# Kernel tuning notes

Measured on AMD Instinct MI355X. Metric: run time of the kernel, lower is better.

Reference implementation:

```python
import jax, jax.numpy as jnp
import numpy as np

N = 40000   # num nodes
C = 128     # in_channels
H = 8       # num_heads
D = C // H  # head_dim = 16
E = 640000  # num edges
FF = 4 * C


def layer_norm(x, g, b, eps=1e-5):
    m = jnp.mean(x, axis=-1, keepdims=True)
    v = jnp.mean((x - m) ** 2, axis=-1, keepdims=True)
    return (x - m) / jnp.sqrt(v + eps) * g + b


def setup_inputs() -> dict:
    key = jax.random.key(0)
    ks = jax.random.split(key, 16)
    s = 0.02
    x = jax.random.normal(ks[0], (N, C), dtype=jnp.float32)
    edge_index = jax.random.randint(ks[1], (2, E), 0, N, dtype=jnp.int64)
    return {
        'x': x,
        'edge_index': edge_index,
        'Wq': jax.random.normal(ks[2], (C, C), jnp.float32) * s,
        'bq': jnp.zeros((C,), jnp.float32),
        'Wk': jax.random.normal(ks[3], (C, C), jnp.float32) * s,
        'bk': jnp.zeros((C,), jnp.float32),
        'Wv': jax.random.normal(ks[4], (C, C), jnp.float32) * s,
        'bv': jnp.zeros((C,), jnp.float32),
        'Wo': jax.random.normal(ks[5], (C, C), jnp.float32) * s,
        'bo': jnp.zeros((C,), jnp.float32),
        'ln1_g': jnp.ones((C,), jnp.float32),
        'ln1_b': jnp.zeros((C,), jnp.float32),
        'ln2_g': jnp.ones((C,), jnp.float32),
        'ln2_b': jnp.zeros((C,), jnp.float32),
        'W1': jax.random.normal(ks[6], (C, FF), jnp.float32) * s,
        'b1': jnp.zeros((FF,), jnp.float32),
        'W2': jax.random.normal(ks[7], (FF, C), jnp.float32) * s,
        'b2': jnp.zeros((C,), jnp.float32),
    }


def reference(x, edge_index, Wq, bq, Wk, bk, Wv, bv, Wo, bo,
              ln1_g, ln1_b, ln2_g, ln2_b, W1, b1, W2, b2):
    residual = x
    xn = layer_norm(x, ln1_g, ln1_b)
    q = (xn @ Wq + bq).reshape(N, H, D)
    k = (xn @ Wk + bk).reshape(N, H, D)
    v = (xn @ Wv + bv).reshape(N, H, D)
    src, dst = edge_index[0], edge_index[1]
    # per-edge scores: [E, H]
    scores = jnp.einsum('ehd,ehd->eh', q[dst], k[src]) / jnp.sqrt(jnp.float32(D))
    # NOTE: faithful to the source — softmax over ALL edges (dim=0), not per-destination
    attn = jax.nn.softmax(scores, axis=0)[:, :, None]          # [E, H, 1]
    weighted = v[src] * attn                                   # [E, H, D]
    aggregated = jax.ops.segment_sum(weighted, dst, num_segments=N)  # [N, H, D]
    out = aggregated.reshape(N, C) @ Wo + bo
    x1 = residual + out
    residual2 = x1
    xn2 = layer_norm(x1, ln2_g, ln2_b)
    ffn = jax.nn.relu(xn2 @ W1 + b1) @ W2 + b2
    return residual2 + ffn
```

## Files before the change

kernel.cpp:

```cpp
#include <hip/hip_runtime.h>
#include <math.h>

#define NNODES 40000
#define CCH    128
#define NH     8
#define HD     16
#define NEDGE  640000
#define NBLK   157
#define FBLK   10000
#define RBLK   40

typedef __attribute__((ext_vector_type(8))) short bf16x8;
typedef __attribute__((ext_vector_type(4))) float f32x4;
typedef __attribute__((ext_vector_type(2))) float f32x2;

__device__ inline unsigned short f2bf(float f) {
  union { float f; unsigned u; } c; c.f = f;
  unsigned r = c.u + 0x7fffu + ((c.u >> 16) & 1u);
  return (unsigned short)(r >> 16);
}
__device__ inline float bfs(unsigned short u) { union { unsigned i; float f; } c; c.i = (unsigned)u << 16; return c.f; }
__device__ inline float bflo(unsigned u) { union { unsigned i; float f; } c; c.i = u << 16; return c.f; }
__device__ inline float bfhi(unsigned u) { union { unsigned i; float f; } c; c.i = u & 0xffff0000u; return c.f; }

__device__ inline unsigned char f2fp8(float v) {
#if __has_builtin(__builtin_amdgcn_cvt_pk_fp8_f32)
  return (unsigned char)(__builtin_amdgcn_cvt_pk_fp8_f32(v, v, 0, false) & 0xff);
#else
  union { float f; unsigned u; } c; c.f = v;
  unsigned s = (c.u >> 24) & 0x80;
  int e = (int)((c.u >> 23) & 0xff) - 127;
  unsigned m = c.u & 0x7fffff;
  if (e > 8) return s | 0x7e;
  if (e >= -6) {
    unsigned q = (m + 0x80000) >> 20; unsigned ee = e + 7;
    if (q == 8) { q = 0; ee++; }
    if (ee > 15) return s | 0x7e;
    return s | (ee << 3) | q;
  }
  if (e < -10) return (unsigned char)s;
  float a = fabsf(v); unsigned q = (unsigned)(a * 512.f + 0.5f); if (q > 7) q = 7;
  return s | q;
#endif
}
__device__ inline void fp8x4d(unsigned w, float* o) {
#if __has_builtin(__builtin_amdgcn_cvt_pk_f32_fp8)
  f32x2 lo = __builtin_amdgcn_cvt_pk_f32_fp8((int)w, false);
  f32x2 hi = __builtin_amdgcn_cvt_pk_f32_fp8((int)w, true);
  o[0] = lo[0]; o[1] = lo[1]; o[2] = hi[0]; o[3] = hi[1];
#else
  #pragma unroll
  for (int i = 0; i < 4; i++) {
    unsigned b = (w >> (8 * i)) & 0xff;
    unsigned s = b >> 7, e = (b >> 3) & 15, m = b & 7;
    float v;
    if (e) { union { unsigned u; float f; } c; c.u = ((e + 120) << 23) | (m << 20); v = c.f; }
    else v = m * (1.f / 512.f);
    o[i] = s ? -v : v;
  }
#endif
}

__global__ __launch_bounds__(256) void k_wprep_all(const float* __restrict__ Wq,
                                                   const float* __restrict__ Wk,
                                                   const float* __restrict__ Wv,
                                                   const float* __restrict__ W1,
                                                   const float* __restrict__ W2,
                                                   const float* __restrict__ bq,
                                                   const float* __restrict__ bk,
                                                   const float* __restrict__ bv,
                                                   unsigned short* __restrict__ Wqkvt,
                                                   unsigned short* __restrict__ W1t,
                                                   unsigned short* __restrict__ W2t,
                                                   float* __restrict__ bqkv,
                                                   int* __restrict__ deg) {
  int g0 = blockIdx.x * 256 + threadIdx.x;
  if (g0 < NNODES) deg[g0] = 0;
  int idx = g0;
  if (idx < 16384) { int n = idx >> 7, k = idx & 127; Wqkvt[idx] = f2bf(Wq[(size_t)k * 128 + n]); return; }
  idx -= 16384;
  if (idx < 16384) { int n = idx >> 7, k = idx & 127; Wqkvt[16384 + (n << 7) + k] = f2bf(Wk[(size_t)k * 128 + n]); return; }
  idx -= 16384;
  if (idx < 16384) { int n = idx >> 7, k = idx & 127; Wqkvt[32768 + (n << 7) + k] = f2bf(Wv[(size_t)k * 128 + n]); return; }
  idx -= 16384;
  if (idx < 65536) { int n = idx >> 7, k = idx & 127; W1t[idx] = f2bf(W1[(size_t)k * 512 + n]); return; }
  idx -= 65536;
  if (idx < 65536) { int n = idx >> 9, k = idx & 511; W2t[idx] = f2bf(W2[(size_t)k * 128 + n]); return; }
  idx -= 65536;
  if (idx < 384) bqkv[idx] = idx < 128 ? bq[idx] : (idx < 256 ? bk[idx - 128] : bv[idx - 256]);
}

__global__ __launch_bounds__(256) void k_wprep_wo(const float* __restrict__ W,
                                                  const float* __restrict__ dpart,
                                                  unsigned short* __restrict__ Wt) {
  __shared__ float sinv[8];
  if (threadIdx.x < 64) {
    int h = threadIdx.x & 7;
    float s = 0.f;
    for (int r = threadIdx.x >> 3; r < RBLK; r += 8) s += dpart[r * 8 + h];
    #pragma unroll
    for (int d = 8; d < 64; d <<= 1) s += __shfl_xor(s, d);
    if (threadIdx.x < 8) sinv[h] = 1.0f / s;
  }
  __syncthreads();
  int idx = blockIdx.x * 256 + threadIdx.x;
  if (idx >= CCH * CCH) return;
  int n = idx >> 7, k = idx & 127;
  Wt[idx] = f2bf(W[(size_t)k * CCH + n] * sinv[k >> 4]);
}

template <int NT, int OUTMODE, bool LNA, bool RELU>
__global__ __launch_bounds__(256) void k_gemm128(const void* __restrict__ Ain,
                                                 const unsigned short* __restrict__ Bt,
                                                 const float* __restrict__ bias,
                                                 const float* __restrict__ lng,
                                                 const float* __restrict__ lnb,
                                                 void* __restrict__ outp) {
  __shared__ unsigned short As[64 * 128];
  __shared__ unsigned short Bs[128 * 128];
  const int tid  = threadIdx.x;
  const int row0 = blockIdx.x * 64;
  const int l    = tid & 63;
  const int w    = tid >> 6;
  const int wr   = w >> 1;
  const int wc   = w & 1;

  if (LNA) {
    const float* x = (const float*)Ain;
    int r = tid >> 2, qt = tid & 3;
    const float4* xr = (const float4*)(x + (size_t)(row0 + r) * 128 + qt * 32);
    float4 xv[8];
    float s = 0.f, ss = 0.f;
    #pragma unroll
    for (int i = 0; i < 8; i++) {
      xv[i] = xr[i];
      s  += xv[i].x + xv[i].y + xv[i].z + xv[i].w;
      ss += xv[i].x * xv[i].x + xv[i].y * xv[i].y + xv[i].z * xv[i].z + xv[i].w * xv[i].w;
    }
    s += __shfl_xor(s, 1); ss += __shfl_xor(ss, 1);
    s += __shfl_xor(s, 2); ss += __shfl_xor(ss, 2);
    float mean = s * (1.f / 128.f);
    float var  = ss * (1.f / 128.f) - mean * mean;
    float rstd = rsqrtf(var + 1e-5f);
    #pragma unroll
    for (int i = 0; i < 8; i += 2) {
      int c0 = qt * 32 + i * 4;
      float va[8] = {xv[i].x, xv[i].y, xv[i].z, xv[i].w,
                     xv[i+1].x, xv[i+1].y, xv[i+1].z, xv[i+1].w};
      unsigned short tmp[8];
      #pragma unroll
      for (int u = 0; u < 8; u++)
        tmp[u] = f2bf((va[u] - mean) * rstd * lng[c0 + u] + lnb[c0 + u]);
      int slot = c0 >> 3;
      *(uint4*)(As + r * 128 + ((slot ^ (r & 7)) * 8)) = *(uint4*)tmp;
    }
  } else {
    const unsigned short* A = (const unsigned short*)Ain;
    #pragma unroll
    for (int it = 0; it < 4; it++) {
      int idx = it * 256 + tid;
      int r = idx >> 4, sl = idx & 15;
      uint4 vv = *(const uint4*)(A + (size_t)(row0 + r) * 128 + sl * 8);
      *(uint4*)(As + r * 128 + ((sl ^ (r & 7)) * 8)) = vv;
    }
  }

  #pragma unroll
  for (int t = 0; t < NT; t++) {
    __syncthreads();
    #pragma unroll
    for (int it = 0; it < 8; it++) {
      int idx = it * 256 + tid;
      int n = idx >> 4, sl = idx & 15;
      uint4 vv = *(const uint4*)(Bt + (size_t)(t * 128 + n) * 128 + sl * 8);
      *(uint4*)(Bs + n * 128 + ((sl ^ (n & 7)) * 8)) = vv;
    }
    __syncthreads();

    f32x4 acc[2][4] = {};
    #pragma unroll
    for (int kk = 0; kk < 4; kk++) {
      int sb = kk * 4 + (l >> 4);
      bf16x8 af[2], bfr[4];
      #pragma unroll
      for (int mi = 0; mi < 2; mi++) {
        int r = wr * 32 + mi * 16 + (l & 15);
        af[mi] = *(const bf16x8*)(As + r * 128 + ((sb ^ (r & 7)) * 8));
      }
      #pragma unroll
      for (int ni = 0; ni < 4; ni++) {
        int n = wc * 64 + ni * 16 + (l & 15);
        bfr[ni] = *(const bf16x8*)(Bs + n * 128 + ((sb ^ (n & 7)) * 8));
      }
      #pragma unroll
      for (int mi = 0; mi < 2; mi++)
        #pragma unroll
        for (int ni = 0; ni < 4; ni++)
          acc[mi][ni] = __builtin_amdgcn_mfma_f32_16x16x32_bf16(af[mi], bfr[ni], acc[mi][ni], 0, 0, 0);
    }

    #pragma unroll
    for (int mi = 0; mi < 2; mi++) {
      #pragma unroll
      for (int p = 0; p < 4; p++) {
        int r = row0 + wr * 32 + mi * 16 + (l >> 4) * 4 + p;
        #pragma unroll
        for (int ni = 0; ni < 4; ni++) {
          int cc = wc * 64 + ni * 16 + (l & 15);
          int c  = t * 128 + cc;
          float val = acc[mi][ni][p] + bias[c];
          if (RELU) val = fmaxf(val, 0.f);
          if (OUTMODE == 1) {
            ((unsigned short*)outp)[(size_t)r * (NT * 128) + c] = f2bf(val);
          } else {
            char* rowb = (char*)outp + (size_t)r * 512;
            if (t == 0)      *(unsigned short*)(rowb + cc * 2) = f2bf(val);
            else if (t == 1) *(unsigned char*)(rowb + 256 + cc) = f2fp8(val);
            else             *(unsigned char*)(rowb + 384 + cc) = f2fp8(val);
          }
        }
      }
    }
  }
}

template <bool RELU, int RESMODE, int MODE>
__global__ __launch_bounds__(256) void k_mgemm(const unsigned short* __restrict__ A,
                                               const unsigned short* __restrict__ Bt,
                                               const float* __restrict__ bias,
                                               const void* __restrict__ res,
                                               void* __restrict__ outp,
                                               int K, int Nc,
                                               const float* __restrict__ lng,
                                               const float* __restrict__ lnb,
                                               void* __restrict__ outp2) {
  __shared__ unsigned short As[64 * 64];
  __shared__ unsigned short Bs[128 * 64];
  const int tid  = threadIdx.x;
  const int row0 = blockIdx.x * 64;
  const int c0   = blockIdx.y * 128;
  const int l    = tid & 63;
  const int w    = tid >> 6;
  const int wr   = w >> 1;
  const int wc   = w & 1;

  f32x4 acc[2][4] = {};

  for (int kc = 0; kc < K; kc += 64) {
    __syncthreads();
    #pragma unroll
    for (int it = 0; it < 2; it++) {
      int idx = it * 256 + tid;
      int r = idx >> 3, s = idx & 7;
      uint4 vv = *(const uint4*)(A + (size_t)(row0 + r) * K + kc + s * 8);
      *(uint4*)(As + r * 64 + ((s ^ (r & 7)) * 8)) = vv;
    }
    #pragma unroll
    for (int it = 0; it < 4; it++) {
      int idx = it * 256 + tid;
      int n = idx >> 3, s = idx & 7;
      uint4 vv = *(const uint4*)(Bt + (size_t)(c0 + n) * K + kc + s * 8);
      *(uint4*)(Bs + n * 64 + ((s ^ (n & 7)) * 8)) = vv;
    }
    __syncthreads();
    #pragma unroll
    for (int kk = 0; kk < 2; kk++) {
      int sb = kk * 4 + (l >> 4);
      bf16x8 af[2], bfr[4];
      #pragma unroll
      for (int mi = 0; mi < 2; mi++) {
        int r = wr * 32 + mi * 16 + (l & 15);
        af[mi] = *(const bf16x8*)(As + r * 64 + ((sb ^ (r & 7)) * 8));
      }
      #pragma unroll
      for (int ni = 0; ni < 4; ni++) {
        int n = wc * 64 + ni * 16 + (l & 15);
        bfr[ni] = *(const bf16x8*)(Bs + n * 64 + ((sb ^ (n & 7)) * 8));
      }
      #pragma unroll
      for (int mi = 0; mi < 2; mi++)
        #pragma unroll
        for (int ni = 0; ni < 4; ni++)
          acc[mi][ni] = __builtin_amdgcn_mfma_f32_16x16x32_bf16(af[mi], bfr[ni], acc[mi][ni], 0, 0, 0);
    }
  }

  if constexpr (MODE == 3) {
    __shared__ float lnS[64][2], lnSS[64][2], gS[128], bS[128];
    if (tid < 128) { gS[tid] = lng[tid]; bS[tid] = lnb[tid]; }
    #pragma unroll
    for (int mi = 0; mi < 2; mi++) {
      #pragma unroll
      for (int p = 0; p < 4; p++) {
        int lr = wr * 32 + mi * 16 + (l >> 4) * 4 + p;
        int r  = row0 + lr;
        float s = 0.f, ss = 0.f;
        #pragma unroll
        for (int ni = 0; ni < 4; ni++) {
          int c = wc * 64 + ni * 16 + (l & 15);
          float val = acc[mi][ni][p] + bias[c] + ((const float*)res)[(size_t)r * 128 + c];
          acc[mi][ni][p] = val;
          s += val; ss += val * val;
        }
        #pragma unroll
        for (int d = 1; d < 16; d <<= 1) { s += __shfl_xor(s, d); ss += __shfl_xor(ss, d); }
        if ((l & 15) == 0) { lnS[lr][wc] = s; lnSS[lr][wc] = ss; }
      }
    }
    __syncthreads();
    #pragma unroll
    for (int mi = 0; mi < 2; mi++) {
      #pragma unroll
      for (int p = 0; p < 4; p++) {
        int lr = wr * 32 + mi * 16 + (l >> 4) * 4 + p;
        int r  = row0 + lr;
        float m   = (lnS[lr][0] + lnS[lr][1]) * (1.f / 128.f);
        float var = (lnSS[lr][0] + lnSS[lr][1]) * (1.f / 128.f) - m * m;
        float rstd = rsqrtf(var + 1e-5f);
        #pragma unroll
        for (int ni = 0; ni < 4; ni++) {
          int c = wc * 64 + ni * 16 + (l & 15);
          float val = acc[mi][ni][p];
          ((unsigned short*)outp)[(size_t)r * 128 + c]  = f2bf(val);
          ((unsigned short*)outp2)[(size_t)r * 128 + c] = f2bf((val - m) * rstd * gS[c] + bS[c]);
        }
      }
    }
  } else {
    #pragma unroll
    for (int mi = 0; mi < 2; mi++) {
      #pragma unroll
      for (int p = 0; p < 4; p++) {
        int r = row0 + wr * 32 + mi * 16 + (l >> 4) * 4 + p;
        #pragma unroll
        for (int ni = 0; ni < 4; ni++) {
          int c = c0 + wc * 64 + ni * 16 + (l & 15);
          float val = acc[mi][ni][p] + bias[c];
          if (RESMODE == 1) val += ((const float*)res)[(size_t)r * Nc + c];
          if (RESMODE == 2) val += bfs(((const unsigned short*)res)[(size_t)r * Nc + c]);
          if (RELU) val = fmaxf(val, 0.f);
          ((float*)outp)[(size_t)r * Nc + c] = val;
        }
      }
    }
  }
}

__global__ __launch_bounds__(256) void k_histrank(const int* __restrict__ ei,
                                                  int* __restrict__ deg,
                                                  int* __restrict__ rank) {
  int e = blockIdx.x * 256 + threadIdx.x;
  if (e >= NEDGE) return;
  rank[e] = atomicAdd(&deg[ei[NEDGE + e]], 1);
}

__global__ __launch_bounds__(256) void k_scan3a(const int* __restrict__ deg,
                                                int* __restrict__ bsum) {
  int i = blockIdx.x * 256 + threadIdx.x;
  int d = (i < NNODES) ? deg[i] : 0;
  #pragma unroll
  for (int s = 1; s < 64; s <<= 1) d += __shfl_xor(d, s);
  __shared__ int ws4[4];
  if ((threadIdx.x & 63) == 0) ws4[threadIdx.x >> 6] = d;
  __syncthreads();
  if (threadIdx.x == 0) bsum[blockIdx.x] = ws4[0] + ws4[1] + ws4[2] + ws4[3];
}

__global__ __launch_bounds__(256) void k_scan3b(const int* __restrict__ bsum,
                                                int* __restrict__ bpre) {
  int t = threadIdx.x;
  int d = (t < NBLK) ? bsum[t] : 0;
  int lane = t & 63, wv = t >> 6;
  int incl = d;
  #pragma unroll
  for (int s = 1; s < 64; s <<= 1) { int o = __shfl_up(incl, s); if (lane >= s) incl += o; }
  __shared__ int wsum[4];
  if (lane == 63) wsum[wv] = incl;
  __syncthreads();
  int base = 0;
  for (int w2 = 0; w2 < wv; w2++) base += wsum[w2];
  if (t < NBLK) bpre[t] = base + incl - d;
}

__global__ __launch_bounds__(256) void k_scan3c(const int* __restrict__ deg,
                                                const int* __restrict__ bpre,
                                                int* __restrict__ off) {
  int t = threadIdx.x;
  int i = blockIdx.x * 256 + t;
  int d = (i < NNODES) ? deg[i] : 0;
  int lane = t & 63, wv = t >> 6;
  int incl = d;
  #pragma unroll
  for (int s = 1; s < 64; s <<= 1) { int o = __shfl_up(incl, s); if (lane >= s) incl += o; }
  __shared__ int wsum[4];
  if (lane == 63) wsum[wv] = incl;
  __syncthreads();
  int base = bpre[blockIdx.x];
  for (int w2 = 0; w2 < wv; w2++) base += wsum[w2];
  int ex = base + incl - d;
  if (i < NNODES) off[i] = ex;
  if (i == 0) off[NNODES] = NEDGE;
}

__global__ __launch_bounds__(256) void k_scatter(const int* __restrict__ ei,
                                                 const int* __restrict__ off,
                                                 const int* __restrict__ rank,
                                                 int* __restrict__ srcs) {
  int e = blockIdx.x * 256 + threadIdx.x;
  if (e >= NEDGE) return;
  srcs[off[ei[NEDGE + e]] + rank[e]] = ei[e];
}

__global__ __launch_bounds__(256) void k_fused(const unsigned char* __restrict__ qkv,
                                               const int* __restrict__ off,
                                               const int* __restrict__ srcs,
                                               unsigned* __restrict__ U,
                                               float* __restrict__ hpart) {
  const int wave = threadIdx.x >> 6;
  const int lane = threadIdx.x & 63;
  const int n  = blockIdx.x * 4 + wave;
  const int g  = lane >> 3;
  const int c8 = lane & 7;

  const uint4* qp = (const uint4*)(qkv + (size_t)n * 512 + c8 * 32);
  uint4 qa = qp[0], qb = qp[1];
  float qf[16];
  qf[0]=bflo(qa.x);  qf[1]=bfhi(qa.x);  qf[2]=bflo(qa.y);  qf[3]=bfhi(qa.y);
  qf[4]=bflo(qa.z);  qf[5]=bfhi(qa.z);  qf[6]=bflo(qa.w);  qf[7]=bfhi(qa.w);
  qf[8]=bflo(qb.x);  qf[9]=bfhi(qb.x);  qf[10]=bflo(qb.y); qf[11]=bfhi(qb.y);
  qf[12]=bflo(qb.z); qf[13]=bfhi(qb.z); qf[14]=bflo(qb.w); qf[15]=bfhi(qb.w);

  float acc[16];
  #pragma unroll
  for (int i = 0; i < 16; i++) acc[i] = 0.f;
  float lsum = 0.f;

  const int i0 = off[n], i1 = off[n + 1];
  if (i1 > i0) {
    int j0 = i0 + g; if (j0 >= i1) j0 = i1 - 1;
    int src = srcs[j0];
    const uint4* kp = (const uint4*)(qkv + (size_t)src * 512 + 256 + c8 * 16);
    uint4 kw = kp[0], vw = kp[8];
    for (int jb = i0; jb < i1; jb += 8) {
      uint4 kc = kw, vc = vw;
      bool valid = jb + g < i1;
      int jn = jb + 8;
      if (jn < i1) {
        int j2 = jn + g; if (j2 >= i1) j2 = i1 - 1;
        int srcn = srcs[j2];
        const uint4* kpn = (const uint4*)(qkv + (size_t)srcn * 512 + 256 + c8 * 16);
        kw = kpn[0]; vw = kpn[8];
      }
      float kf[16], vf[16];
      fp8x4d(kc.x, kf + 0); fp8x4d(kc.y, kf + 4); fp8x4d(kc.z, kf + 8); fp8x4d(kc.w, kf + 12);
      fp8x4d(vc.x, vf + 0); fp8x4d(vc.y, vf + 4); fp8x4d(vc.z, vf + 8); fp8x4d(vc.w, vf + 12);
      float p = 0.f;
      #pragma unroll
      for (int i = 0; i < 16; i++) p += qf[i] * kf[i];
      float w = valid ? __expf(p * 0.25f) : 0.f;
      lsum += w;
      #pragma unroll
      for (int i = 0; i < 16; i++) acc[i] += w * vf[i];
    }
  }

  #pragma unroll
  for (int d = 8; d < 64; d <<= 1) {
    #pragma unroll
    for (int i = 0; i < 16; i++) acc[i] += __shfl_xor(acc[i], d);
    lsum += __shfl_xor(lsum, d);
  }

  __shared__ float wsum[4][8];
  if (lane < 8) {
    wsum[wave][c8] = lsum;
    unsigned o[8];
    #pragma unroll
    for (int i = 0; i < 8; i++)
      o[i] = ((unsigned)f2bf(acc[2 * i + 1]) << 16) | f2bf(acc[2 * i]);
    uint4* up = (uint4*)(U + (size_t)n * 64 + c8 * 8);
    up[0] = make_uint4(o[0], o[1], o[2], o[3]);
    up[1] = make_uint4(o[4], o[5], o[6], o[7]);
  }
  __syncthreads();
  if (threadIdx.x < 8) {
    hpart[blockIdx.x * 8 + threadIdx.x] =
        wsum[0][threadIdx.x] + wsum[1][threadIdx.x] + wsum[2][threadIdx.x] + wsum[3][threadIdx.x];
  }
}

__global__ __launch_bounds__(256) void k_reduce_part(const float* __restrict__ hpart,
                                                     float* __restrict__ dpart) {
  const int t = threadIdx.x;
  const int h = t & 7;
  const int r0 = blockIdx.x * (FBLK / RBLK);
  float s = 0.f;
  for (int r = r0 + (t >> 3); r < r0 + FBLK / RBLK; r += 32) s += hpart[r * 8 + h];
  #pragma unroll
  for (int d = 8; d < 64; d <<= 1) s += __shfl_xor(s, d);
  __shared__ float ws4[4][8];
  int lane = t & 63, wv = t >> 6;
  if (lane < 8) ws4[wv][lane] = s;
  __syncthreads();
  if (t < 8) dpart[blockIdx.x * 8 + t] = ws4[0][t] + ws4[1][t] + ws4[2][t] + ws4[3][t];
}

extern "C" void kernel_launch(void* const* d_in, const int* in_sizes, int n_in,
                              void* d_out, int out_size, void* d_ws, size_t ws_size,
                              hipStream_t stream) {
  const float* x    = (const float*)d_in[0];
  const int*   ei   = (const int*)d_in[1];
  const float* Wq   = (const float*)d_in[2];
  const float* bq   = (const float*)d_in[3];
  const float* Wk   = (const float*)d_in[4];
  const float* bk   = (const float*)d_in[5];
  const float* Wv   = (const float*)d_in[6];
  const float* bv   = (const float*)d_in[7];
  const float* Wo   = (const float*)d_in[8];
  const float* bo   = (const float*)d_in[9];
  const float* ln1g = (const float*)d_in[10];
  const float* ln1b = (const float*)d_in[11];
  const float* ln2g = (const float*)d_in[12];
  const float* ln2b = (const float*)d_in[13];
  const float* W1   = (const float*)d_in[14];
  const float* b1   = (const float*)d_in[15];
  const float* W2   = (const float*)d_in[16];
  const float* b2   = (const float*)d_in[17];
  float* out = (float*)d_out;

  char* p = (char*)d_ws;
  const size_t NCb = (size_t)NNODES * CCH * 2;
  unsigned short* xn2  = (unsigned short*)p; p += NCb;
  unsigned char*  qkvb = (unsigned char*)p;  p += (size_t)NNODES * 512;
  unsigned short* agg  = (unsigned short*)p; p += NCb;
  p += NCb;
  unsigned short* x1b  = (unsigned short*)p; p += NCb;
  int* deg    = (int*)p;                     p += (size_t)NNODES * 4 + 256;
  int* off    = (int*)p;                     p += (size_t)(NNODES + 1) * 4 + 256;
  int* rank   = (int*)p;                     p += (size_t)NEDGE * 4;
  int* srcs   = (int*)p;                     p += (size_t)NEDGE * 4;
  int* bsum   = (int*)p;                     p += 256 * 4;
  int* bpre   = (int*)p;                     p += 256 * 4;
  float* hpart = (float*)p;                  p += (size_t)FBLK * 8 * 4;
  float* dpart = (float*)p;                  p += (size_t)RBLK * 8 * 4 + 256;
  float* bqkv  = (float*)p;                  p += 384 * 4 + 256;
  unsigned short* Wqkvt = (unsigned short*)p; p += (size_t)384 * CCH * 2;
  unsigned short* Wot   = (unsigned short*)p; p += (size_t)CCH * CCH * 2;
  unsigned short* W1t   = (unsigned short*)p; p += (size_t)CCH * 4 * CCH * 2;
  unsigned short* W2t   = (unsigned short*)p; p += (size_t)CCH * 4 * CCH * 2;
  unsigned short* ffn1 = (unsigned short*)qkvb;

  dim3 blk(256);
  dim3 gM(NNODES / 64, 1);
  dim3 gE((NEDGE + 255) / 256);

  k_wprep_all<<<706, blk, 0, stream>>>(Wq, Wk, Wv, W1, W2, bq, bk, bv,
                                       Wqkvt, W1t, W2t, bqkv, deg);

  k_histrank<<<gE, blk, 0, stream>>>(ei, deg, rank);
  k_scan3a<<<NBLK, blk, 0, stream>>>(deg, bsum);
  k_scan3b<<<1, blk, 0, stream>>>(bsum, bpre);
  k_scan3c<<<NBLK, blk, 0, stream>>>(deg, bpre, off);
  k_scatter<<<gE, blk, 0, stream>>>(ei, off, rank, srcs);

  k_gemm128<3, 2, true, false><<<gM, blk, 0, stream>>>(x, Wqkvt, bqkv,
                                                       ln1g, ln1b, qkvb);

  k_fused<<<FBLK, blk, 0, stream>>>(qkvb, off, srcs, (unsigned*)agg, hpart);
  k_reduce_part<<<RBLK, blk, 0, stream>>>(hpart, dpart);

  k_wprep_wo<<<64, blk, 0, stream>>>(Wo, dpart, Wot);
  k_mgemm<false, 1, 3><<<gM, blk, 0, stream>>>(agg, Wot, bo, x, x1b,
                                               CCH, CCH, ln2g, ln2b, xn2);

  k_gemm128<4, 1, false, true><<<gM, blk, 0, stream>>>(xn2, W1t, b1,
                                                       nullptr, nullptr, ffn1);
  k_mgemm<false, 2, 0><<<gM, blk, 0, stream>>>(ffn1, W2t, b2, x1b, out,
                                               4 * CCH, CCH, nullptr, nullptr, nullptr);
}
```

Baseline: 161.4 us.

## Merge block-prefix scan into offset kernel, coarsen edge kernels, deepen src prefetch

The single-block scan kernel is removed. Each block of the offset kernel now sums the preceding block totals itself, which saves one launch. The histogram and scatter kernels each process four edges per thread with a quarter of the blocks. The attention gather loop now loads source indices two iterations ahead, so the index load is off the critical path of the K/V gather, at the cost of a few extra registers.

```diff
diff --git a/kernel.cpp b/kernel.cpp
--- a/kernel.cpp
+++ b/kernel.cpp
@@ -9,6 +9,7 @@
 #define NBLK   157
 #define FBLK   10000
 #define RBLK   40
+#define EBLK   625
 
 typedef __attribute__((ext_vector_type(8))) short bf16x8;
 typedef __attribute__((ext_vector_type(4))) float f32x4;
@@ -349,9 +350,12 @@
 __global__ __launch_bounds__(256) void k_histrank(const int* __restrict__ ei,
                                                   int* __restrict__ deg,
                                                   int* __restrict__ rank) {
-  int e = blockIdx.x * 256 + threadIdx.x;
-  if (e >= NEDGE) return;
-  rank[e] = atomicAdd(&deg[ei[NEDGE + e]], 1);
+  int base = blockIdx.x * 1024 + threadIdx.x;
+  #pragma unroll
+  for (int u = 0; u < 4; u++) {
+    int e = base + u * 256;
+    if (e < NEDGE) rank[e] = atomicAdd(&deg[ei[NEDGE + e]], 1);
+  }
 }
 
 __global__ __launch_bounds__(256) void k_scan3a(const int* __restrict__ deg,
@@ -366,37 +370,33 @@
   if (threadIdx.x == 0) bsum[blockIdx.x] = ws4[0] + ws4[1] + ws4[2] + ws4[3];
 }
 
-__global__ __launch_bounds__(256) void k_scan3b(const int* __restrict__ bsum,
-                                                int* __restrict__ bpre) {
-  int t = threadIdx.x;
-  int d = (t < NBLK) ? bsum[t] : 0;
-  int lane = t & 63, wv = t >> 6;
-  int incl = d;
-  #pragma unroll
-  for (int s = 1; s < 64; s <<= 1) { int o = __shfl_up(incl, s); if (lane >= s) incl += o; }
-  __shared__ int wsum[4];
-  if (lane == 63) wsum[wv] = incl;
-  __syncthreads();
-  int base = 0;
-  for (int w2 = 0; w2 < wv; w2++) base += wsum[w2];
-  if (t < NBLK) bpre[t] = base + incl - d;
-}
-
 __global__ __launch_bounds__(256) void k_scan3c(const int* __restrict__ deg,
-                                                const int* __restrict__ bpre,
+                                                const int* __restrict__ bsum,
                                                 int* __restrict__ off) {
-  int t = threadIdx.x;
+  const int t = threadIdx.x;
+  __shared__ int ws4[4];
+  __shared__ int sbase;
+  {
+    int lim = blockIdx.x < NBLK ? blockIdx.x : NBLK;
+    int v = (t < lim) ? bsum[t] : 0;
+    #pragma unroll
+    for (int s = 1; s < 64; s <<= 1) v += __shfl_xor(v, s);
+    if ((t & 63) == 0) ws4[t >> 6] = v;
+    __syncthreads();
+    if (t == 0) sbase = ws4[0] + ws4[1] + ws4[2] + ws4[3];
+    __syncthreads();
+  }
   int i = blockIdx.x * 256 + t;
   int d = (i < NNODES) ? deg[i] : 0;
   int lane = t & 63, wv = t >> 6;
   int incl = d;
   #pragma unroll
   for (int s = 1; s < 64; s <<= 1) { int o = __shfl_up(incl, s); if (lane >= s) incl += o; }
-  __shared__ int wsum[4];
-  if (lane == 63) wsum[wv] = incl;
   __syncthreads();
-  int base = bpre[blockIdx.x];
-  for (int w2 = 0; w2 < wv; w2++) base += wsum[w2];
+  if (lane == 63) ws4[wv] = incl;
+  __syncthreads();
+  int base = sbase;
+  for (int w2 = 0; w2 < wv; w2++) base += ws4[w2];
   int ex = base + incl - d;
   if (i < NNODES) off[i] = ex;
   if (i == 0) off[NNODES] = NEDGE;
@@ -406,9 +406,12 @@
                                                  const int* __restrict__ off,
                                                  const int* __restrict__ rank,
                                                  int* __restrict__ srcs) {
-  int e = blockIdx.x * 256 + threadIdx.x;
-  if (e >= NEDGE) return;
-  srcs[off[ei[NEDGE + e]] + rank[e]] = ei[e];
+  int base = blockIdx.x * 1024 + threadIdx.x;
+  #pragma unroll
+  for (int u = 0; u < 4; u++) {
+    int e = base + u * 256;
+    if (e < NEDGE) srcs[off[ei[NEDGE + e]] + rank[e]] = ei[e];
+  }
 }
 
 __global__ __launch_bounds__(256) void k_fused(const unsigned char* __restrict__ qkv,
@@ -438,18 +441,27 @@
   const int i0 = off[n], i1 = off[n + 1];
   if (i1 > i0) {
     int j0 = i0 + g; if (j0 >= i1) j0 = i1 - 1;
-    int src = srcs[j0];
-    const uint4* kp = (const uint4*)(qkv + (size_t)src * 512 + 256 + c8 * 16);
-    uint4 kw = kp[0], vw = kp[8];
+    int sA = srcs[j0];
+    int sB;
+    {
+      int j1 = i0 + 8 + g;
+      if (j1 >= i1) j1 = i1 - 1;
+      sB = srcs[j1];
+    }
+    const uint4* kpA = (const uint4*)(qkv + (size_t)sA * 512 + 256 + c8 * 16);
+    uint4 kw = kpA[0], vw = kpA[8];
+
     for (int jb = i0; jb < i1; jb += 8) {
       uint4 kc = kw, vc = vw;
       bool valid = jb + g < i1;
-      int jn = jb + 8;
-      if (jn < i1) {
-        int j2 = jn + g; if (j2 >= i1) j2 = i1 - 1;
-        int srcn = srcs[j2];
-        const uint4* kpn = (const uint4*)(qkv + (size_t)srcn * 512 + 256 + c8 * 16);
-        kw = kpn[0]; vw = kpn[8];
+      if (jb + 8 < i1) {
+        const uint4* kpB = (const uint4*)(qkv + (size_t)sB * 512 + 256 + c8 * 16);
+        kw = kpB[0]; vw = kpB[8];
+      }
+      if (jb + 16 < i1) {
+        int j2 = jb + 16 + g;
+        if (j2 >= i1) j2 = i1 - 1;
+        sB = srcs[j2];
       }
       float kf[16], vf[16];
       fp8x4d(kc.x, kf + 0); fp8x4d(kc.y, kf + 4); fp8x4d(kc.z, kf + 8); fp8x4d(kc.w, kf + 12);
@@ -540,7 +552,6 @@
   int* rank   = (int*)p;                     p += (size_t)NEDGE * 4;
   int* srcs   = (int*)p;                     p += (size_t)NEDGE * 4;
   int* bsum   = (int*)p;                     p += 256 * 4;
-  int* bpre   = (int*)p;                     p += 256 * 4;
   float* hpart = (float*)p;                  p += (size_t)FBLK * 8 * 4;
   float* dpart = (float*)p;                  p += (size_t)RBLK * 8 * 4 + 256;
   float* bqkv  = (float*)p;                  p += 384 * 4 + 256;
@@ -552,16 +563,14 @@
 
   dim3 blk(256);
   dim3 gM(NNODES / 64, 1);
-  dim3 gE((NEDGE + 255) / 256);
 
   k_wprep_all<<<706, blk, 0, stream>>>(Wq, Wk, Wv, W1, W2, bq, bk, bv,
                                        Wqkvt, W1t, W2t, bqkv, deg);
 
-  k_histrank<<<gE, blk, 0, stream>>>(ei, deg, rank);
+  k_histrank<<<EBLK, blk, 0, stream>>>(ei, deg, rank);
   k_scan3a<<<NBLK, blk, 0, stream>>>(deg, bsum);
-  k_scan3b<<<1, blk, 0, stream>>>(bsum, bpre);
-  k_scan3c<<<NBLK, blk, 0, stream>>>(deg, bpre, off);
-  k_scatter<<<gE, blk, 0, stream>>>(ei, off, rank, srcs);
+  k_scan3c<<<NBLK, blk, 0, stream>>>(deg, bsum, off);
+  k_scatter<<<EBLK, blk, 0, stream>>>(ei, off, rank, srcs);
 
   k_gemm128<3, 2, true, false><<<gM, blk, 0, stream>>>(x, Wqkvt, bqkv,
                                                        ln1g, ln1b, qkvb);
```

After: 156.5 us. 3.0% less time.
